# Performance work log

Hardware: AMD Instinct MI355X
Metric: run time of the kernel (lower is better)

The kernel has to match this reference:

```python
import jax, jax.numpy as jnp
import numpy as np

H = 128; W = 128          # BEV grid (row_num_embed = col_num_embed = 128)
B = 1
CIN = 384; D = 256; NH = 8; NP = 4; NF = 128  # NF = num_feats of pos encoding
NLAYERS = 4               # 3 cross + 1 self


def setup_inputs() -> dict:
    key = jax.random.key(0)
    ks = jax.random.split(key, 32)
    s = 0.02
    rn = lambda k, shp: (jax.random.normal(k, shp, dtype=jnp.float32) * s)
    z = lambda shp: jnp.zeros(shp, jnp.float32)
    inp = {
        'query': jax.random.normal(ks[0], (B, CIN, H, W), jnp.float32),
        'value': jax.random.normal(ks[1], (B, CIN, H, W), jnp.float32),
        # 1x1 conv input projections (out, in)
        'conv_q_w': rn(ks[2], (D, CIN)), 'conv_q_b': z((D,)),
        'conv_v_w': rn(ks[3], (D, CIN)), 'conv_v_b': z((D,)),
        # learned positional embedding tables
        'row_embed': rn(ks[4], (H, NF)), 'col_embed': rn(ks[5], (W, NF)),
        # pre-attention linear layers (in, out)
        'lin_q_w': rn(ks[6], (D, D)), 'lin_q_b': z((D,)),
        'lin_v_w': rn(ks[7], (D, D)), 'lin_v_b': z((D,)),
        # stacked MSDeformAttn params for 4 layers
        'msda_off_w': rn(ks[8], (NLAYERS, D, NH * NP * 2)), 'msda_off_b': z((NLAYERS, NH * NP * 2)),
        'msda_aw_w': rn(ks[9], (NLAYERS, D, NH * NP)), 'msda_aw_b': z((NLAYERS, NH * NP)),
        'msda_vp_w': rn(ks[10], (NLAYERS, D, D)), 'msda_vp_b': z((NLAYERS, D)),
        'msda_op_w': rn(ks[11], (NLAYERS, D, D)), 'msda_op_b': z((NLAYERS, D)),
        # output MLP: 256 -> 128 -> 64 -> 384 with LayerNorm+ReLU between
        'out_w1': rn(ks[12], (D, D // 2)), 'out_b1': z((D // 2,)),
        'ln1_g': jnp.ones((D // 2,), jnp.float32), 'ln1_b': z((D // 2,)),
        'out_w2': rn(ks[13], (D // 2, D // 4)), 'out_b2': z((D // 4,)),
        'ln2_g': jnp.ones((D // 4,), jnp.float32), 'ln2_b': z((D // 4,)),
        'out_w3': rn(ks[14], (D // 4, CIN)), 'out_b3': z((CIN,)),
    }
    return inp


def _ln(x, g, b):
    mu = jnp.mean(x, -1, keepdims=True)
    var = jnp.mean(jnp.square(x - mu), -1, keepdims=True)
    return (x - mu) * jax.lax.rsqrt(var + 1e-5) * g + b


def reference(query, value, conv_q_w, conv_q_b, conv_v_w, conv_v_b, row_embed, col_embed,
              lin_q_w, lin_q_b, lin_v_w, lin_v_b,
              msda_off_w, msda_off_b, msda_aw_w, msda_aw_b,
              msda_vp_w, msda_vp_b, msda_op_w, msda_op_b,
              out_w1, out_b1, ln1_g, ln1_b, out_w2, out_b2, ln2_g, ln2_b, out_w3, out_b3):
    Bv, Cin, Hh, Ww = query.shape
    Nq = Hh * Ww
    HD = D // NH
    # 1x1 convs = per-pixel channel matmul; layout (Nq, B, D) = flatten(2).permute(2,0,1)
    q = jnp.einsum('bchw,dc->hwbd', query, conv_q_w).reshape(Nq, Bv, D) + conv_q_b
    v = jnp.einsum('bchw,dc->hwbd', value, conv_v_w).reshape(Nq, Bv, D) + conv_v_b
    # LearnedPositionalEncoding: cat([col_embed(x), row_embed(y)], -1)
    pos = jnp.concatenate([
        jnp.broadcast_to(col_embed[None, :Ww], (Hh, Ww, NF)),
        jnp.broadcast_to(row_embed[:Hh, None], (Hh, Ww, NF))], -1).reshape(Nq, 1, D)
    q = q @ lin_q_w + lin_q_b
    v = v @ lin_v_w + lin_v_b
    # reference points (pixel centers, normalized, (x, y) order)
    ry = (jnp.arange(Hh, dtype=q.dtype) + 0.5) / Hh
    rx = (jnp.arange(Ww, dtype=q.dtype) + 0.5) / Ww
    gx, gy = jnp.meshgrid(rx, ry, indexing='xy')  # (H, W)
    ref = jnp.stack([gx, gy], -1).reshape(1, Nq, 2)
    inv_wh = jnp.array([1.0 / Ww, 1.0 / Hh], dtype=q.dtype)

    def msda_layer(q_in, v_in, i):
        qp = q_in + pos                                   # query + query_pos
        val = (v_in @ msda_vp_w[i] + msda_vp_b[i]).transpose(1, 0, 2).reshape(Bv, Hh, Ww, NH, HD)
        off = (qp @ msda_off_w[i] + msda_off_b[i]).transpose(1, 0, 2).reshape(Bv, Nq, NH, NP, 2)
        aw = jax.nn.softmax((qp @ msda_aw_w[i] + msda_aw_b[i]).transpose(1, 0, 2)
                            .reshape(Bv, Nq, NH, NP), axis=-1)
        loc = ref[:, :, None, None, :] + off * inv_wh     # (B, Nq, NH, NP, 2) in [0,1]
        # bilinear sampling, zero padding, align_corners=False (grid_sample semantics)
        x = loc[..., 0] * Ww - 0.5
        y = loc[..., 1] * Hh - 0.5
        x0f = jnp.floor(x); y0f = jnp.floor(y)
        lx = (x - x0f).transpose(0, 2, 1, 3)              # (B, NH, Nq, NP)
        ly = (y - y0f).transpose(0, 2, 1, 3)
        x0 = x0f.astype(jnp.int32).transpose(0, 2, 1, 3)
        y0 = y0f.astype(jnp.int32).transpose(0, 2, 1, 3)
        vflat = val.transpose(0, 3, 1, 2, 4).reshape(Bv, NH, Hh * Ww, HD)
        awt = aw.transpose(0, 2, 1, 3)                    # (B, NH, Nq, NP)

        def corner(yi, xi, w):
            valid = (yi >= 0) & (yi < Hh) & (xi >= 0) & (xi < Ww)
            idx = (jnp.clip(yi, 0, Hh - 1) * Ww + jnp.clip(xi, 0, Ww - 1)).reshape(Bv, NH, Nq * NP, 1)
            g = jnp.take_along_axis(vflat, idx, axis=2).reshape(Bv, NH, Nq, NP, HD)
            return g * (w * valid.astype(w.dtype) * awt)[..., None]

        out = (corner(y0, x0, (1 - lx) * (1 - ly))
               + corner(y0, x0 + 1, lx * (1 - ly))
               + corner(y0 + 1, x0, (1 - lx) * ly)
               + corner(y0 + 1, x0 + 1, lx * ly)).sum(3)  # (B, NH, Nq, HD)
        out = out.transpose(2, 0, 1, 3).reshape(Nq, Bv, D)
        return out @ msda_op_w[i] + msda_op_b[i] + q_in   # residual (dropout=identity, eval)

    for i in range(3):                                    # cross layers: value features
        q = msda_layer(q, v, i)
    q = msda_layer(q, q, 3)                               # self layer: value = query

    h1 = jax.nn.relu(_ln(q @ out_w1 + out_b1, ln1_g, ln1_b))
    h2 = jax.nn.relu(_ln(h1 @ out_w2 + out_b2, ln2_g, ln2_b))
    out = h2 @ out_w3 + out_b3                            # (Nq, B, Cin)
    return out.transpose(1, 2, 0).reshape(Bv, Cin, Hh, Ww)
```

## Files before the change

kernel.cpp:

```cpp
#include <hip/hip_runtime.h>
#include <hip/hip_bf16.h>

#define NQ   16384
#define DIM  256

using bf16 = __hip_bfloat16;
using bf16x8 = __attribute__((ext_vector_type(8))) short;
using f32x4  = __attribute__((ext_vector_type(4))) float;

__device__ __forceinline__ float b2f(bf16 x) { return __bfloat162float(x); }
__device__ __forceinline__ bf16  f2b(float x) { return __float2bfloat16(x); }
__device__ __forceinline__ unsigned short f2bb(float x) {
    bf16 h = __float2bfloat16(x);
    return *(unsigned short*)&h;
}
__device__ __forceinline__ float us2f(unsigned short u) {
    unsigned int x = ((unsigned int)u) << 16;
    return __builtin_bit_cast(float, x);
}

__device__ __forceinline__ void xcd_map(int& sx, int& sy)
{
    const int gx  = gridDim.x;
    const int nwg = gridDim.x * gridDim.y;
    const int bid = blockIdx.y * gx + blockIdx.x;
    const int q = nwg >> 3, r = nwg & 7;
    const int xcd = bid & 7, sl = bid >> 3;
    const int s = (xcd < r ? xcd * (q + 1) : r * (q + 1) + (xcd - r) * q) + sl;
    sx = s % gx;
    sy = s / gx;
}

template<int MW, int NF, int KS>
__device__ __forceinline__ void gcore(
    bf16* __restrict__ Bs,
    const bf16* __restrict__ A, const bf16* __restrict__ Bgl,
    const float* __restrict__ bias, const bf16* __restrict__ res,
    const float* __restrict__ ce, const float* __restrict__ re,
    bf16* __restrict__ C, bf16* __restrict__ C2,
    int N, int n0, int m0)
{
    constexpr int K   = KS * 32;
    constexpr int LDB = K + 8;

    const int t    = threadIdx.x;
    const int lane = t & 63;
    const int wid  = t >> 6;
    const int lr   = lane & 15;
    const int lg   = lane >> 4;

    const bf16* Ab = A + (size_t)(m0 + wid * MW * 16 + lr) * K + lg * 8;

    bf16x8 af0[MW], af1[MW], af2[MW];
#pragma unroll
    for (int mi = 0; mi < MW; ++mi)
        af0[mi] = *(const bf16x8*)&Ab[(size_t)(mi * 16) * K + 0];
    if (KS > 1) {
#pragma unroll
        for (int mi = 0; mi < MW; ++mi)
            af1[mi] = *(const bf16x8*)&Ab[(size_t)(mi * 16) * K + 32];
    }

#pragma unroll
    for (int c = 0; c < NF * KS / 4; ++c) {
        const int id  = c * 256 + t;
        const int row = id / (KS * 4);
        const int kc  = id % (KS * 4);
        *(int4*)&Bs[row * LDB + kc * 8] = *(const int4*)&Bgl[(size_t)row * K + kc * 8];
    }
    __syncthreads();

    f32x4 acc[MW][NF];
#pragma unroll
    for (int i = 0; i < MW; ++i)
#pragma unroll
        for (int j = 0; j < NF; ++j) {
            f32x4 z = {0.f, 0.f, 0.f, 0.f};
            acc[i][j] = z;
        }

    bf16x8 bcur[NF], bnxt[NF];
#pragma unroll
    for (int jj = 0; jj < NF; ++jj)
        bcur[jj] = *(const bf16x8*)&Bs[(jj * 16 + lr) * LDB + lg * 8];

#pragma unroll
    for (int s = 0; s < KS; ++s) {
        if (s + 2 < KS) {
#pragma unroll
            for (int mi = 0; mi < MW; ++mi)
                af2[mi] = *(const bf16x8*)&Ab[(size_t)(mi * 16) * K + (s + 2) * 32];
        }
        if (s + 1 < KS) {
#pragma unroll
            for (int jj = 0; jj < NF; ++jj)
                bnxt[jj] = *(const bf16x8*)&Bs[(jj * 16 + lr) * LDB + (s + 1) * 32 + lg * 8];
        }
#pragma unroll
        for (int mi = 0; mi < MW; ++mi)
#pragma unroll
            for (int jj = 0; jj < NF; ++jj)
                acc[mi][jj] = __builtin_amdgcn_mfma_f32_16x16x32_bf16(
                    af0[mi], bcur[jj], acc[mi][jj], 0, 0, 0);
#pragma unroll
        for (int mi = 0; mi < MW; ++mi) { af0[mi] = af1[mi]; af1[mi] = af2[mi]; }
#pragma unroll
        for (int jj = 0; jj < NF; ++jj) bcur[jj] = bnxt[jj];
    }

    const bool dores = res != nullptr;
    const bool doqp  = C2 != nullptr;
#pragma unroll
    for (int mi = 0; mi < MW; ++mi) {
#pragma unroll
        for (int jj = 0; jj < NF; ++jj) {
            const int row0 = m0 + wid * MW * 16 + mi * 16 + lg * 4;
            const int col  = n0 + jj * 16 + lr;
            const float bvl = bias[col];
#pragma unroll
            for (int r = 0; r < 4; ++r) {
                const size_t off = (size_t)(row0 + r) * N + col;
                float v = acc[mi][jj][r] + bvl;
                if (dores) v += b2f(res[off]);
                C[off] = f2b(v);
                if (doqp) {
                    const int row = row0 + r;
                    const float pv = (col < 128)
                        ? ce[(row & 127) * 128 + col]
                        : re[(row >> 7) * 128 + (col - 128)];
                    C2[(size_t)row * 256 + col] = f2b(v + pv);
                }
            }
        }
    }
}

template<int MW, int KS>
__global__ __launch_bounds__(256)
void gmm_std(const bf16* __restrict__ A, const bf16* __restrict__ B,
             const float* __restrict__ bias, const bf16* __restrict__ res,
             const float* __restrict__ ce, const float* __restrict__ re,
             bf16* __restrict__ C, bf16* __restrict__ C2, int N)
{
    __shared__ bf16 Bs[64 * (KS * 32 + 8)];
    int sx, sy;
    xcd_map(sx, sy);
    const int n0 = sx * 64;
    gcore<MW, 4, KS>(Bs, A, B + (size_t)n0 * (KS * 32), bias, res, ce, re, C, C2,
                     N, n0, sy * (MW * 64));
}

__global__ __launch_bounds__(256)
void gmm_qv(const bf16* __restrict__ QT, const bf16* __restrict__ WQ,
            const float* __restrict__ BQ, bf16* __restrict__ QA, bf16* __restrict__ QPb,
            const bf16* __restrict__ VT, const bf16* __restrict__ WV,
            const float* __restrict__ BV, bf16* __restrict__ V,
            const float* __restrict__ ce, const float* __restrict__ re)
{
    __shared__ bf16 Bs[64 * (384 + 8)];
    int sx, sy;
    xcd_map(sx, sy);
    const int m0 = sy * 128;
    if (sx < 4) {
        const int n0 = sx * 64;
        gcore<2, 4, 12>(Bs, QT, WQ + (size_t)n0 * 384, BQ, nullptr, ce, re,
                        QA, QPb, 256, n0, m0);
    } else {
        const int n0 = (sx - 4) * 64;
        gcore<2, 4, 12>(Bs, VT, WV + (size_t)n0 * 384, BV, nullptr, nullptr, nullptr,
                        V, nullptr, 256, n0, m0);
    }
}

__global__ __launch_bounds__(256)
void gmm_vpall(const bf16* __restrict__ V, const bf16* __restrict__ WVP,
               const float* __restrict__ vp_b, bf16* __restrict__ VP,
               const bf16* __restrict__ QPb, const bf16* __restrict__ Boa,
               const float* __restrict__ boa, bf16* __restrict__ OA)
{
    __shared__ bf16 Bs[64 * (256 + 8)];
    int sx, sy;
    xcd_map(sx, sy);
    const int m0 = sy * 64;
    if (sx < 12) {
        const int layer = sx >> 2;
        const int nloc  = (sx & 3) * 64;
        gcore<1, 4, 8>(Bs, V, WVP + (size_t)sx * 64 * 256,
                       vp_b + layer * 256, nullptr, nullptr, nullptr,
                       VP + (size_t)layer * NQ * 256, nullptr, 256, nloc, m0);
    } else {
        const int n0 = (sx - 12) * 64;
        gcore<1, 4, 8>(Bs, QPb, Boa + (size_t)n0 * 256, boa, nullptr, nullptr, nullptr,
                       OA, nullptr, 128, n0, m0);
    }
}

__global__ __launch_bounds__(256)
void gmm_vo3(const bf16* __restrict__ cur, const bf16* __restrict__ Bvp,
             const float* __restrict__ bvp, bf16* __restrict__ T2,
             const bf16* __restrict__ QPb, const bf16* __restrict__ Boa,
             const float* __restrict__ boa, bf16* __restrict__ OA)
{
    __shared__ bf16 Bs[64 * (256 + 8)];
    int sx, sy;
    xcd_map(sx, sy);
    const int m0 = sy * 64;
    if (sx < 4) {
        const int n0 = sx * 64;
        gcore<1, 4, 8>(Bs, cur, Bvp + (size_t)n0 * 256, bvp, nullptr, nullptr, nullptr,
                       T2, nullptr, 256, n0, m0);
    } else {
        const int n0 = (sx - 4) * 64;
        gcore<1, 4, 8>(Bs, QPb, Boa + (size_t)n0 * 256, boa, nullptr, nullptr, nullptr,
                       OA, nullptr, 128, n0, m0);
    }
}

__global__ __launch_bounds__(256)
void gmm_out(const bf16* __restrict__ A, const bf16* __restrict__ B,
             const float* __restrict__ bias, float* __restrict__ out)
{
    constexpr int KS = 2, K = 64, LDB = K + 8;
    __shared__ bf16 Bs[64 * LDB];
    int sx, sy;
    xcd_map(sx, sy);
    const int n0 = sx * 64;
    const int m0 = sy * 64;

    const int t    = threadIdx.x;
    const int lane = t & 63;
    const int wid  = t >> 6;
    const int lr   = lane & 15;
    const int lg   = lane >> 4;

    const bf16* Ab = A + (size_t)(m0 + wid * 16 + lr) * K + lg * 8;
    const bf16* Bb = B + (size_t)n0 * K;

    bf16x8 af0 = *(const bf16x8*)&Ab[0];
    bf16x8 af1 = *(const bf16x8*)&Ab[32];

#pragma unroll
    for (int c = 0; c < 2; ++c) {
        const int id  = c * 256 + t;
        const int row = id >> 3, kc = id & 7;
        *(int4*)&Bs[row * LDB + kc * 8] = *(const int4*)&Bb[(size_t)row * K + kc * 8];
    }
    __syncthreads();

    f32x4 acc[4];
#pragma unroll
    for (int j = 0; j < 4; ++j) { f32x4 z = {0.f, 0.f, 0.f, 0.f}; acc[j] = z; }

#pragma unroll
    for (int s = 0; s < KS; ++s) {
        const bf16x8 af = s == 0 ? af0 : af1;
#pragma unroll
        for (int jj = 0; jj < 4; ++jj) {
            const bf16x8 bf = *(const bf16x8*)&Bs[(jj * 16 + lr) * LDB + s * 32 + lg * 8];
            acc[jj] = __builtin_amdgcn_mfma_f32_16x16x32_bf16(af, bf, acc[jj], 0, 0, 0);
        }
    }

    const int row0 = m0 + wid * 16 + lg * 4;
#pragma unroll
    for (int jj = 0; jj < 4; ++jj) {
        const int col = n0 + jj * 16 + lr;
        const float bvl = bias[col];
        float4 o;
        o.x = acc[jj][0] + bvl;
        o.y = acc[jj][1] + bvl;
        o.z = acc[jj][2] + bvl;
        o.w = acc[jj][3] + bvl;
        *(float4*)&out[(size_t)col * NQ + row0] = o;
    }
}

template<int NF, int KS>
__device__ __forceinline__ void gcore_ln(
    bf16* __restrict__ Bs,
    const bf16* __restrict__ A, const bf16* __restrict__ Bgl,
    const float* __restrict__ bias, bf16* __restrict__ C,
    const float* __restrict__ lng, const float* __restrict__ lnb,
    int N, int m0)
{
    constexpr int K    = KS * 32;
    constexpr int LDB  = K + 8;
    constexpr int NPAN = NF * 16;

    const int t    = threadIdx.x;
    const int lane = t & 63;
    const int wid  = t >> 6;
    const int lr   = lane & 15;
    const int lg   = lane >> 4;

#pragma unroll
    for (int c = 0; c < NF * KS / 4; ++c) {
        const int id  = c * 256 + t;
        const int row = id / (KS * 4);
        const int kc  = id % (KS * 4);
        *(int4*)&Bs[row * LDB + kc * 8] = *(const int4*)&Bgl[(size_t)row * K + kc * 8];
    }
    __syncthreads();

    f32x4 acc[NF];
#pragma unroll
    for (int j = 0; j < NF; ++j) { f32x4 z = {0.f, 0.f, 0.f, 0.f}; acc[j] = z; }

    const bf16* Ab = A + (size_t)(m0 + wid * 16 + lr) * K + lg * 8;

#pragma unroll
    for (int s = 0; s < KS; ++s) {
        bf16x8 af = *(const bf16x8*)&Ab[s * 32];
#pragma unroll
        for (int jj = 0; jj < NF; ++jj) {
            const bf16x8 bf = *(const bf16x8*)&Bs[(jj * 16 + lr) * LDB + s * 32 + lg * 8];
            acc[jj] = __builtin_amdgcn_mfma_f32_16x16x32_bf16(af, bf, acc[jj], 0, 0, 0);
        }
    }

    float bvl[NF], gv[NF], bb[NF];
#pragma unroll
    for (int jj = 0; jj < NF; ++jj) {
        const int col = jj * 16 + lr;
        bvl[jj] = bias[col]; gv[jj] = lng[col]; bb[jj] = lnb[col];
    }
#pragma unroll
    for (int r = 0; r < 4; ++r) {
        float v[NF];
        float s = 0.f;
#pragma unroll
        for (int jj = 0; jj < NF; ++jj) { v[jj] = acc[jj][r] + bvl[jj]; s += v[jj]; }
        s += __shfl_xor(s, 1); s += __shfl_xor(s, 2);
        s += __shfl_xor(s, 4); s += __shfl_xor(s, 8);
        const float mu = s * (1.f / NPAN);
        float vs = 0.f;
#pragma unroll
        for (int jj = 0; jj < NF; ++jj) { const float d = v[jj] - mu; vs += d * d; }
        vs += __shfl_xor(vs, 1); vs += __shfl_xor(vs, 2);
        vs += __shfl_xor(vs, 4); vs += __shfl_xor(vs, 8);
        const float rstd = rsqrtf(vs * (1.f / NPAN) + 1e-5f);
        const int row = m0 + wid * 16 + lg * 4 + r;
#pragma unroll
        for (int jj = 0; jj < NF; ++jj) {
            const float o = (v[jj] - mu) * rstd * gv[jj] + bb[jj];
            C[(size_t)row * N + jj * 16 + lr] = f2b(fmaxf(o, 0.f));
        }
    }
}

__global__ __launch_bounds__(256)
void gmm_mlp1(const bf16* __restrict__ A, const bf16* __restrict__ B,
              const float* __restrict__ bias, bf16* __restrict__ C,
              const float* __restrict__ g, const float* __restrict__ b)
{
    __shared__ bf16 Bs[128 * (256 + 8)];
    gcore_ln<8, 8>(Bs, A, B, bias, C, g, b, 128, blockIdx.y * 64);
}

__global__ __launch_bounds__(256)
void gmm_mlp2(const bf16* __restrict__ A, const bf16* __restrict__ B,
              const float* __restrict__ bias, bf16* __restrict__ C,
              const float* __restrict__ g, const float* __restrict__ b)
{
    __shared__ bf16 Bs[64 * (128 + 8)];
    gcore_ln<4, 4>(Bs, A, B, bias, C, g, b, 64, blockIdx.y * 64);
}

__global__ __launch_bounds__(256)
void prep_all(const float* __restrict__ query, const float* __restrict__ value,
              bf16* __restrict__ QT, bf16* __restrict__ VT,
              const float* __restrict__ vp_w, const float* __restrict__ op_w,
              const float* __restrict__ off_w, const float* __restrict__ aw_w,
              const float* __restrict__ off_b, const float* __restrict__ aw_b,
              const float* __restrict__ w1, const float* __restrict__ w2,
              const float* __restrict__ w3,
              bf16* __restrict__ WVP, bf16* __restrict__ WOP, bf16* __restrict__ WOA,
              bf16* __restrict__ WM1, bf16* __restrict__ WM2, bf16* __restrict__ WM3,
              float* __restrict__ OAB,
              const float* __restrict__ cqw, const float* __restrict__ cqb,
              const float* __restrict__ cvw, const float* __restrict__ cvb,
              const float* __restrict__ lqw, const float* __restrict__ lqb,
              const float* __restrict__ lvw, const float* __restrict__ lvb,
              bf16* __restrict__ WQc, bf16* __restrict__ WVc,
              float* __restrict__ BQc, float* __restrict__ BVc)
{
    __shared__ float tile2[2][64][65];
    const int b = blockIdx.x;
    const int t = threadIdx.x;
    const int tr  = t >> 4;
    const int tc4 = (t & 15) * 4;

    if (b < 1536) {
        const int z = b / 768, rem = b % 768;
        const float* in = z ? value : query;
        bf16* out = z ? VT : QT;
        const int c0 = (rem % 6) * 64, m0 = (rem / 6) * 128;
#pragma unroll
        for (int i = 0; i < 4; ++i) {
            const int c = i * 16 + tr;
            const size_t base = (size_t)(c0 + c) * NQ + m0 + tc4;
            const float4 va = *(const float4*)&in[base];
            const float4 vb = *(const float4*)&in[base + 64];
            tile2[0][tc4 + 0][c] = va.x; tile2[0][tc4 + 1][c] = va.y;
            tile2[0][tc4 + 2][c] = va.z; tile2[0][tc4 + 3][c] = va.w;
            tile2[1][tc4 + 0][c] = vb.x; tile2[1][tc4 + 1][c] = vb.y;
            tile2[1][tc4 + 2][c] = vb.z; tile2[1][tc4 + 3][c] = vb.w;
        }
        __syncthreads();
#pragma unroll
        for (int i = 0; i < 4; ++i) {
            const int m = i * 16 + tr;
            ushort4 oa, ob;
            oa.x = f2bb(tile2[0][m][tc4 + 0]); oa.y = f2bb(tile2[0][m][tc4 + 1]);
            oa.z = f2bb(tile2[0][m][tc4 + 2]); oa.w = f2bb(tile2[0][m][tc4 + 3]);
            ob.x = f2bb(tile2[1][m][tc4 + 0]); ob.y = f2bb(tile2[1][m][tc4 + 1]);
            ob.z = f2bb(tile2[1][m][tc4 + 2]); ob.w = f2bb(tile2[1][m][tc4 + 3]);
            *(ushort4*)&out[(size_t)(m0 + m) * 384 + c0 + tc4] = oa;
            *(ushort4*)&out[(size_t)(m0 + 64 + m) * 384 + c0 + tc4] = ob;
        }
        return;
    }
    if (b < 1712) {
        const int ti = b - 1536;
        const float* src; bf16* dst; int K, N, k0, n0, Nt;
        if (ti < 64)       { const int l = ti >> 4, r = ti & 15; src = vp_w + l * 65536; dst = WVP + l * 65536; K = 256; N = 256; k0 = (r >> 2) * 64; n0 = (r & 3) * 64; Nt = 64; }
        else if (ti < 128) { const int l = (ti - 64) >> 4, r = (ti - 64) & 15; src = op_w + l * 65536; dst = WOP + l * 65536; K = 256; N = 256; k0 = (r >> 2) * 64; n0 = (r & 3) * 64; Nt = 64; }
        else if (ti < 144) { const int l = (ti - 128) >> 2, r = (ti - 128) & 3; src = off_w + l * 16384; dst = WOA + l * 32768; K = 256; N = 64; k0 = r * 64; n0 = 0; Nt = 64; }
        else if (ti < 160) { const int l = (ti - 144) >> 2, r = (ti - 144) & 3; src = aw_w + l * 8192; dst = WOA + l * 32768 + 16384; K = 256; N = 32; k0 = r * 64; n0 = 0; Nt = 32; }
        else if (ti < 168) { const int r = ti - 160; src = w1; dst = WM1; K = 256; N = 128; k0 = (r >> 1) * 64; n0 = (r & 1) * 64; Nt = 64; }
        else if (ti < 170) { const int r = ti - 168; src = w2; dst = WM2; K = 128; N = 64; k0 = r * 64; n0 = 0; Nt = 64; }
        else               { const int r = ti - 170; src = w3; dst = WM3; K = 64; N = 384; k0 = 0; n0 = r * 64; Nt = 64; }
#pragma unroll
        for (int i = 0; i < 4; ++i) {
            const int k = i * 16 + tr;
            if (tc4 < Nt) {
                const float4 vv = *(const float4*)&src[(size_t)(k0 + k) * N + n0 + tc4];
                tile2[0][k][tc4 + 0] = vv.x; tile2[0][k][tc4 + 1] = vv.y;
                tile2[0][k][tc4 + 2] = vv.z; tile2[0][k][tc4 + 3] = vv.w;
            }
        }
        __syncthreads();
#pragma unroll
        for (int i = 0; i < 4; ++i) {
            const int n = i * 16 + tr;
            if (n < Nt) {
                ushort4 o;
                o.x = f2bb(tile2[0][tc4 + 0][n]); o.y = f2bb(tile2[0][tc4 + 1][n]);
                o.z = f2bb(tile2[0][tc4 + 2][n]); o.w = f2bb(tile2[0][tc4 + 3][n]);
                *(ushort4*)&dst[(size_t)(n0 + n) * K + k0 + tc4] = o;
            }
        }
        return;
    }
    if (b < 1728) {
        const int z0 = (b - 1712) * 2048 + t * 8;
        const int l = z0 >> 13, r = z0 & 8191;
        bf16x8 zz = {0, 0, 0, 0, 0, 0, 0, 0};
        *(bf16x8*)&WOA[(size_t)l * 32768 + 24576 + r] = zz;
        return;
    }
    if (b < 2497) {
        const int bb = b - 1728;
        if (bb < 768) {
            const bool isq = bb < 384;
            const float* cw = isq ? cqw : cvw;
            const float* lw = isq ? lqw : lvw;
            bf16* W = isq ? WQc : WVc;
            const int idx = (bb % 384) * 256 + t;
            const int n = idx / 384, c = idx % 384;
            float s = 0.f;
            for (int d = 0; d < 256; ++d)
                s = fmaf(cw[d * 384 + c], lw[d * 256 + n], s);
            W[idx] = f2b(s);
        } else {
            const int n = t;
            float sq = lqb[n], sv = lvb[n];
            for (int d = 0; d < 256; ++d) {
                sq = fmaf(cqb[d], lqw[d * 256 + n], sq);
                sv = fmaf(cvb[d], lvw[d * 256 + n], sv);
            }
            BQc[n] = sq; BVc[n] = sv;
        }
        return;
    }
    {
        const int idx = (b - 2497) * 256 + t;
        if (idx < 512) {
            const int l = idx >> 7, r = idx & 127;
            OAB[idx] = (r < 64) ? off_b[l * 64 + r] : (r < 96 ? aw_b[l * 32 + r - 64] : 0.f);
        }
    }
}

__global__ __launch_bounds__(256)
void sample_kernel(const bf16* __restrict__ val, const bf16* __restrict__ oa,
                   bf16* __restrict__ out)
{
    const int tid = threadIdx.x;
    const int pix = blockIdx.x * 8 + (tid >> 5);
    const int thr = tid & 31;
    const int head = thr >> 2;
    const int c0 = thr * 8;
    const float fx = (float)(pix & 127);
    const float fy = (float)(pix >> 7);
    const unsigned short* oap = (const unsigned short*)(oa + (size_t)pix * 128);
    const bf16x8 offs = *(const bf16x8*)&oap[head * 8];
    const ushort4 lg4 = *(const ushort4*)&oap[64 + head * 4];
    const float l0 = us2f(lg4.x), l1 = us2f(lg4.y), l2 = us2f(lg4.z), l3 = us2f(lg4.w);
    const float mx = fmaxf(fmaxf(l0, l1), fmaxf(l2, l3));
    const float e0 = __expf(l0 - mx), e1 = __expf(l1 - mx);
    const float e2 = __expf(l2 - mx), e3 = __expf(l3 - mx);
    const float inv = 1.f / (e0 + e1 + e2 + e3);
    const float aw4[4] = {e0 * inv, e1 * inv, e2 * inv, e3 * inv};

    float acc[8];
#pragma unroll
    for (int c = 0; c < 8; ++c) acc[c] = 0.f;

#pragma unroll
    for (int p = 0; p < 4; ++p) {
        const float x = fx + us2f((unsigned short)offs[p * 2 + 0]);
        const float y = fy + us2f((unsigned short)offs[p * 2 + 1]);
        const float x0f = floorf(x), y0f = floorf(y);
        const float lx = x - x0f, ly = y - y0f;
        const int x0 = (int)x0f, y0 = (int)y0f;
        const float a = aw4[p];
        const float wc[4] = {(1.f - lx) * (1.f - ly) * a, lx * (1.f - ly) * a,
                             (1.f - lx) * ly * a,         lx * ly * a};
        const int xs[4] = {x0, x0 + 1, x0, x0 + 1};
        const int ys[4] = {y0, y0, y0 + 1, y0 + 1};
#pragma unroll
        for (int k = 0; k < 4; ++k) {
            if ((unsigned)ys[k] < 128u && (unsigned)xs[k] < 128u) {
                const bf16x8 v = *(const bf16x8*)&val[(size_t)((ys[k] << 7) + xs[k]) * 256 + c0];
                const float w = wc[k];
#pragma unroll
                for (int c = 0; c < 8; ++c)
                    acc[c] = fmaf(us2f((unsigned short)v[c]), w, acc[c]);
            }
        }
    }
    bf16x8 o;
#pragma unroll
    for (int c = 0; c < 8; ++c) o[c] = (short)f2bb(acc[c]);
    *(bf16x8*)&out[(size_t)pix * 256 + c0] = o;
}

extern "C" void kernel_launch(void* const* d_in, const int* in_sizes, int n_in,
                              void* d_out, int out_size, void* d_ws, size_t ws_size,
                              hipStream_t stream)
{
    const float* query     = (const float*)d_in[0];
    const float* value     = (const float*)d_in[1];
    const float* conv_q_w  = (const float*)d_in[2];
    const float* conv_q_b  = (const float*)d_in[3];
    const float* conv_v_w  = (const float*)d_in[4];
    const float* conv_v_b  = (const float*)d_in[5];
    const float* row_embed = (const float*)d_in[6];
    const float* col_embed = (const float*)d_in[7];
    const float* lin_q_w   = (const float*)d_in[8];
    const float* lin_q_b   = (const float*)d_in[9];
    const float* lin_v_w   = (const float*)d_in[10];
    const float* lin_v_b   = (const float*)d_in[11];
    const float* off_w     = (const float*)d_in[12];
    const float* off_b     = (const float*)d_in[13];
    const float* aw_w      = (const float*)d_in[14];
    const float* aw_b      = (const float*)d_in[15];
    const float* vp_w      = (const float*)d_in[16];
    const float* vp_b      = (const float*)d_in[17];
    const float* op_w      = (const float*)d_in[18];
    const float* op_b      = (const float*)d_in[19];
    const float* out_w1    = (const float*)d_in[20];
    const float* out_b1    = (const float*)d_in[21];
    const float* ln1_g     = (const float*)d_in[22];
    const float* ln1_b     = (const float*)d_in[23];
    const float* out_w2    = (const float*)d_in[24];
    const float* out_b2    = (const float*)d_in[25];
    const float* ln2_g     = (const float*)d_in[26];
    const float* ln2_b     = (const float*)d_in[27];
    const float* out_w3    = (const float*)d_in[28];
    const float* out_b3    = (const float*)d_in[29];

    bf16* w = (bf16*)d_ws;
    auto alloc = [&](size_t n) { bf16* p = w; w += n; return p; };
    bf16* QT  = alloc((size_t)NQ * 384);
    bf16* VT  = alloc((size_t)NQ * 384);
    bf16* QA  = alloc((size_t)NQ * 256);
    bf16* QB  = alloc((size_t)NQ * 256);
    bf16* QPb = alloc((size_t)NQ * 256);
    bf16* V   = alloc((size_t)NQ * 256);
    bf16* T1  = alloc((size_t)NQ * 256);
    bf16* T2  = alloc((size_t)NQ * 256);
    bf16* VP  = alloc((size_t)3 * NQ * 256);
    bf16* OA  = alloc((size_t)NQ * 128);
    bf16* WQc = alloc(256 * 384);
    bf16* WVc = alloc(256 * 384);
    bf16* WVP = alloc(4 * 256 * 256);
    bf16* WOP = alloc(4 * 256 * 256);
    bf16* WOA = alloc(4 * 128 * 256);
    bf16* WM1 = alloc(128 * 256);
    bf16* WM2 = alloc(64 * 128);
    bf16* WM3 = alloc(384 * 64);
    float* fp = (float*)w;
    float* BQc = fp; fp += 256;
    float* BVc = fp; fp += 256;
    float* OAB = fp; fp += 512;

    const dim3 blk(256);

    prep_all<<<2499, blk, 0, stream>>>(
        query, value, QT, VT,
        vp_w, op_w, off_w, aw_w, off_b, aw_b, out_w1, out_w2, out_w3,
        WVP, WOP, WOA, WM1, WM2, WM3, OAB,
        conv_q_w, conv_q_b, conv_v_w, conv_v_b,
        lin_q_w, lin_q_b, lin_v_w, lin_v_b,
        WQc, WVc, BQc, BVc);

    gmm_qv<<<dim3(8, 128), blk, 0, stream>>>(
        QT, WQc, BQc, QA, QPb, VT, WVc, BVc, V, col_embed, row_embed);
    gmm_vpall<<<dim3(14, 256), blk, 0, stream>>>(
        V, WVP, vp_b, VP, QPb, WOA, OAB, OA);

    bf16* cur = QA;
    bf16* nxt = QB;
    for (int i = 0; i < 4; ++i) {
        const bf16* valbuf;
        if (i < 3) {
            valbuf = VP + (size_t)i * NQ * 256;
            if (i > 0)
                gmm_std<1, 8><<<dim3(2, 256), blk, 0, stream>>>(
                    QPb, WOA + (size_t)i * 32768, OAB + i * 128, nullptr,
                    nullptr, nullptr, OA, nullptr, 128);
        } else {
            valbuf = T2;
            gmm_vo3<<<dim3(6, 256), blk, 0, stream>>>(
                cur, WVP + (size_t)3 * 65536, vp_b + 3 * 256, T2,
                QPb, WOA + (size_t)3 * 32768, OAB + 3 * 128, OA);
        }
        sample_kernel<<<2048, blk, 0, stream>>>(valbuf, OA, T1);
        gmm_std<1, 8><<<dim3(4, 256), blk, 0, stream>>>(
            T1, WOP + (size_t)i * 65536, op_b + i * 256, cur,
            col_embed, row_embed, nxt, QPb, 256);
        bf16* tmp = cur; cur = nxt; nxt = tmp;
    }

    gmm_mlp1<<<dim3(1, 256), blk, 0, stream>>>(cur, WM1, out_b1, T1, ln1_g, ln1_b);
    gmm_mlp2<<<dim3(1, 256), blk, 0, stream>>>(T1, WM2, out_b2, T2, ln2_g, ln2_b);
    gmm_out<<<dim3(6, 256), blk, 0, stream>>>(T2, WM3, out_b3, (float*)d_out);
}
```

Measured before the change: 230.7 us.

## Fuse fp32 input transpose/convert into QV projection GEMM A-loads

Removes the prep stage that transposed the fp32 channel-major query/value into bf16 row-major buffers. The QV GEMM now reads fp32 channel-major A directly, packs it to bf16 in registers, and prefetches two k-steps ahead. This drops an extra write and read of two 16384x384 intermediates. The cost is that each GEMM block reads A in fp32, twice the bytes of bf16, and with scalar strided loads. A is also re-read by every N-tile block.

```diff
diff --git a/kernel.cpp b/kernel.cpp
--- a/kernel.cpp
+++ b/kernel.cpp
@@ -17,6 +17,12 @@
 __device__ __forceinline__ float us2f(unsigned short u) {
     unsigned int x = ((unsigned int)u) << 16;
     return __builtin_bit_cast(float, x);
+}
+__device__ __forceinline__ bf16x8 pack8(const float* f) {
+    bf16x8 r;
+#pragma unroll
+    for (int j = 0; j < 8; ++j) r[j] = (short)f2bb(f[j]);
+    return r;
 }
 
 __device__ __forceinline__ void xcd_map(int& sx, int& sy)
@@ -135,6 +141,110 @@
     }
 }
 
+template<int MW, int NF, int KS>
+__device__ __forceinline__ void gcore_f32A(
+    bf16* __restrict__ Bs,
+    const float* __restrict__ A, const bf16* __restrict__ Bgl,
+    const float* __restrict__ bias,
+    const float* __restrict__ ce, const float* __restrict__ re,
+    bf16* __restrict__ C, bf16* __restrict__ C2,
+    int N, int n0, int m0)
+{
+    constexpr int K   = KS * 32;
+    constexpr int LDB = K + 8;
+
+    const int t    = threadIdx.x;
+    const int lane = t & 63;
+    const int wid  = t >> 6;
+    const int lr   = lane & 15;
+    const int lg   = lane >> 4;
+
+    const int rowb = m0 + wid * MW * 16 + lr;
+
+    float fa0[MW][8], fa1[MW][8], fa2[MW][8];
+    auto loadA = [&](float f[MW][8], int s) {
+        const int k0 = s * 32 + lg * 8;
+#pragma unroll
+        for (int mi = 0; mi < MW; ++mi)
+#pragma unroll
+            for (int j = 0; j < 8; ++j)
+                f[mi][j] = A[(size_t)(k0 + j) * NQ + rowb + mi * 16];
+    };
+    loadA(fa0, 0);
+    if (KS > 1) loadA(fa1, 1);
+
+#pragma unroll
+    for (int c = 0; c < NF * KS / 4; ++c) {
+        const int id  = c * 256 + t;
+        const int row = id / (KS * 4);
+        const int kc  = id % (KS * 4);
+        *(int4*)&Bs[row * LDB + kc * 8] = *(const int4*)&Bgl[(size_t)row * K + kc * 8];
+    }
+    __syncthreads();
+
+    f32x4 acc[MW][NF];
+#pragma unroll
+    for (int i = 0; i < MW; ++i)
+#pragma unroll
+        for (int j = 0; j < NF; ++j) {
+            f32x4 z = {0.f, 0.f, 0.f, 0.f};
+            acc[i][j] = z;
+        }
+
+    bf16x8 bcur[NF], bnxt[NF];
+#pragma unroll
+    for (int jj = 0; jj < NF; ++jj)
+        bcur[jj] = *(const bf16x8*)&Bs[(jj * 16 + lr) * LDB + lg * 8];
+
+#pragma unroll
+    for (int s = 0; s < KS; ++s) {
+        if (s + 2 < KS) loadA(fa2, s + 2);
+        if (s + 1 < KS) {
+#pragma unroll
+            for (int jj = 0; jj < NF; ++jj)
+                bnxt[jj] = *(const bf16x8*)&Bs[(jj * 16 + lr) * LDB + (s + 1) * 32 + lg * 8];
+        }
+#pragma unroll
+        for (int mi = 0; mi < MW; ++mi) {
+            const bf16x8 af = pack8(fa0[mi]);
+#pragma unroll
+            for (int jj = 0; jj < NF; ++jj)
+                acc[mi][jj] = __builtin_amdgcn_mfma_f32_16x16x32_bf16(
+                    af, bcur[jj], acc[mi][jj], 0, 0, 0);
+        }
+#pragma unroll
+        for (int mi = 0; mi < MW; ++mi)
+#pragma unroll
+            for (int j = 0; j < 8; ++j) { fa0[mi][j] = fa1[mi][j]; fa1[mi][j] = fa2[mi][j]; }
+#pragma unroll
+        for (int jj = 0; jj < NF; ++jj) bcur[jj] = bnxt[jj];
+    }
+
+    const bool doqp = C2 != nullptr;
+#pragma unroll
+    for (int mi = 0; mi < MW; ++mi) {
+#pragma unroll
+        for (int jj = 0; jj < NF; ++jj) {
+            const int row0 = m0 + wid * MW * 16 + mi * 16 + lg * 4;
+            const int col  = n0 + jj * 16 + lr;
+            const float bvl = bias[col];
+#pragma unroll
+            for (int r = 0; r < 4; ++r) {
+                const size_t off = (size_t)(row0 + r) * N + col;
+                float v = acc[mi][jj][r] + bvl;
+                C[off] = f2b(v);
+                if (doqp) {
+                    const int row = row0 + r;
+                    const float pv = (col < 128)
+                        ? ce[(row & 127) * 128 + col]
+                        : re[(row >> 7) * 128 + (col - 128)];
+                    C2[(size_t)row * 256 + col] = f2b(v + pv);
+                }
+            }
+        }
+    }
+}
+
 template<int MW, int KS>
 __global__ __launch_bounds__(256)
 void gmm_std(const bf16* __restrict__ A, const bf16* __restrict__ B,
@@ -151,9 +261,9 @@
 }
 
 __global__ __launch_bounds__(256)
-void gmm_qv(const bf16* __restrict__ QT, const bf16* __restrict__ WQ,
+void gmm_qv(const float* __restrict__ Qf, const bf16* __restrict__ WQ,
             const float* __restrict__ BQ, bf16* __restrict__ QA, bf16* __restrict__ QPb,
-            const bf16* __restrict__ VT, const bf16* __restrict__ WV,
+            const float* __restrict__ Vf, const bf16* __restrict__ WV,
             const float* __restrict__ BV, bf16* __restrict__ V,
             const float* __restrict__ ce, const float* __restrict__ re)
 {
@@ -163,12 +273,12 @@
     const int m0 = sy * 128;
     if (sx < 4) {
         const int n0 = sx * 64;
-        gcore<2, 4, 12>(Bs, QT, WQ + (size_t)n0 * 384, BQ, nullptr, ce, re,
-                        QA, QPb, 256, n0, m0);
+        gcore_f32A<2, 4, 12>(Bs, Qf, WQ + (size_t)n0 * 384, BQ, ce, re,
+                             QA, QPb, 256, n0, m0);
     } else {
         const int n0 = (sx - 4) * 64;
-        gcore<2, 4, 12>(Bs, VT, WV + (size_t)n0 * 384, BV, nullptr, nullptr, nullptr,
-                        V, nullptr, 256, n0, m0);
+        gcore_f32A<2, 4, 12>(Bs, Vf, WV + (size_t)n0 * 384, BV, nullptr, nullptr,
+                             V, nullptr, 256, n0, m0);
     }
 }
 
@@ -367,9 +477,7 @@
 }
 
 __global__ __launch_bounds__(256)
-void prep_all(const float* __restrict__ query, const float* __restrict__ value,
-              bf16* __restrict__ QT, bf16* __restrict__ VT,
-              const float* __restrict__ vp_w, const float* __restrict__ op_w,
+void prep_all(const float* __restrict__ vp_w, const float* __restrict__ op_w,
               const float* __restrict__ off_w, const float* __restrict__ aw_w,
               const float* __restrict__ off_b, const float* __restrict__ aw_b,
               const float* __restrict__ w1, const float* __restrict__ w2,
@@ -384,44 +492,14 @@
               bf16* __restrict__ WQc, bf16* __restrict__ WVc,
               float* __restrict__ BQc, float* __restrict__ BVc)
 {
-    __shared__ float tile2[2][64][65];
+    __shared__ float tile[64][65];
     const int b = blockIdx.x;
     const int t = threadIdx.x;
     const int tr  = t >> 4;
     const int tc4 = (t & 15) * 4;
 
-    if (b < 1536) {
-        const int z = b / 768, rem = b % 768;
-        const float* in = z ? value : query;
-        bf16* out = z ? VT : QT;
-        const int c0 = (rem % 6) * 64, m0 = (rem / 6) * 128;
-#pragma unroll
-        for (int i = 0; i < 4; ++i) {
-            const int c = i * 16 + tr;
-            const size_t base = (size_t)(c0 + c) * NQ + m0 + tc4;
-            const float4 va = *(const float4*)&in[base];
-            const float4 vb = *(const float4*)&in[base + 64];
-            tile2[0][tc4 + 0][c] = va.x; tile2[0][tc4 + 1][c] = va.y;
-            tile2[0][tc4 + 2][c] = va.z; tile2[0][tc4 + 3][c] = va.w;
-            tile2[1][tc4 + 0][c] = vb.x; tile2[1][tc4 + 1][c] = vb.y;
-            tile2[1][tc4 + 2][c] = vb.z; tile2[1][tc4 + 3][c] = vb.w;
-        }
-        __syncthreads();
-#pragma unroll
-        for (int i = 0; i < 4; ++i) {
-            const int m = i * 16 + tr;
-            ushort4 oa, ob;
-            oa.x = f2bb(tile2[0][m][tc4 + 0]); oa.y = f2bb(tile2[0][m][tc4 + 1]);
-            oa.z = f2bb(tile2[0][m][tc4 + 2]); oa.w = f2bb(tile2[0][m][tc4 + 3]);
-            ob.x = f2bb(tile2[1][m][tc4 + 0]); ob.y = f2bb(tile2[1][m][tc4 + 1]);
-            ob.z = f2bb(tile2[1][m][tc4 + 2]); ob.w = f2bb(tile2[1][m][tc4 + 3]);
-            *(ushort4*)&out[(size_t)(m0 + m) * 384 + c0 + tc4] = oa;
-            *(ushort4*)&out[(size_t)(m0 + 64 + m) * 384 + c0 + tc4] = ob;
-        }
-        return;
-    }
-    if (b < 1712) {
-        const int ti = b - 1536;
+    if (b < 176) {
+        const int ti = b;
         const float* src; bf16* dst; int K, N, k0, n0, Nt;
         if (ti < 64)       { const int l = ti >> 4, r = ti & 15; src = vp_w + l * 65536; dst = WVP + l * 65536; K = 256; N = 256; k0 = (r >> 2) * 64; n0 = (r & 3) * 64; Nt = 64; }
         else if (ti < 128) { const int l = (ti - 64) >> 4, r = (ti - 64) & 15; src = op_w + l * 65536; dst = WOP + l * 65536; K = 256; N = 256; k0 = (r >> 2) * 64; n0 = (r & 3) * 64; Nt = 64; }
@@ -435,8 +513,8 @@
             const int k = i * 16 + tr;
             if (tc4 < Nt) {
                 const float4 vv = *(const float4*)&src[(size_t)(k0 + k) * N + n0 + tc4];
-                tile2[0][k][tc4 + 0] = vv.x; tile2[0][k][tc4 + 1] = vv.y;
-                tile2[0][k][tc4 + 2] = vv.z; tile2[0][k][tc4 + 3] = vv.w;
+                tile[k][tc4 + 0] = vv.x; tile[k][tc4 + 1] = vv.y;
+                tile[k][tc4 + 2] = vv.z; tile[k][tc4 + 3] = vv.w;
             }
         }
         __syncthreads();
@@ -445,22 +523,22 @@
             const int n = i * 16 + tr;
             if (n < Nt) {
                 ushort4 o;
-                o.x = f2bb(tile2[0][tc4 + 0][n]); o.y = f2bb(tile2[0][tc4 + 1][n]);
-                o.z = f2bb(tile2[0][tc4 + 2][n]); o.w = f2bb(tile2[0][tc4 + 3][n]);
+                o.x = f2bb(tile[tc4 + 0][n]); o.y = f2bb(tile[tc4 + 1][n]);
+                o.z = f2bb(tile[tc4 + 2][n]); o.w = f2bb(tile[tc4 + 3][n]);
                 *(ushort4*)&dst[(size_t)(n0 + n) * K + k0 + tc4] = o;
             }
         }
         return;
     }
-    if (b < 1728) {
-        const int z0 = (b - 1712) * 2048 + t * 8;
+    if (b < 192) {
+        const int z0 = (b - 176) * 2048 + t * 8;
         const int l = z0 >> 13, r = z0 & 8191;
         bf16x8 zz = {0, 0, 0, 0, 0, 0, 0, 0};
         *(bf16x8*)&WOA[(size_t)l * 32768 + 24576 + r] = zz;
         return;
     }
-    if (b < 2497) {
-        const int bb = b - 1728;
+    if (b < 961) {
+        const int bb = b - 192;
         if (bb < 768) {
             const bool isq = bb < 384;
             const float* cw = isq ? cqw : cvw;
@@ -484,7 +562,7 @@
         return;
     }
     {
-        const int idx = (b - 2497) * 256 + t;
+        const int idx = (b - 961) * 256 + t;
         if (idx < 512) {
             const int l = idx >> 7, r = idx & 127;
             OAB[idx] = (r < 64) ? off_b[l * 64 + r] : (r < 96 ? aw_b[l * 32 + r - 64] : 0.f);
@@ -583,8 +661,6 @@
 
     bf16* w = (bf16*)d_ws;
     auto alloc = [&](size_t n) { bf16* p = w; w += n; return p; };
-    bf16* QT  = alloc((size_t)NQ * 384);
-    bf16* VT  = alloc((size_t)NQ * 384);
     bf16* QA  = alloc((size_t)NQ * 256);
     bf16* QB  = alloc((size_t)NQ * 256);
     bf16* QPb = alloc((size_t)NQ * 256);
@@ -608,8 +684,7 @@
 
     const dim3 blk(256);
 
-    prep_all<<<2499, blk, 0, stream>>>(
-        query, value, QT, VT,
+    prep_all<<<963, blk, 0, stream>>>(
         vp_w, op_w, off_w, aw_w, off_b, aw_b, out_w1, out_w2, out_w3,
         WVP, WOP, WOA, WM1, WM2, WM3, OAB,
         conv_q_w, conv_q_b, conv_v_w, conv_v_b,
@@ -617,7 +692,7 @@
         WQc, WVc, BQc, BVc);
 
     gmm_qv<<<dim3(8, 128), blk, 0, stream>>>(
-        QT, WQc, BQc, QA, QPb, VT, WVc, BVc, V, col_embed, row_embed);
+        query, WQc, BQc, QA, QPb, value, WVc, BVc, V, col_embed, row_embed);
     gmm_vpall<<<dim3(14, 256), blk, 0, stream>>>(
         V, WVP, vp_b, VP, QPb, WOA, OAB, OA);
 
```

Measured after the change: 222.7 us. 3.5% less time.
